# Performance work log

Hardware: AMD Instinct MI355X
Metric: run time of the kernel (lower is better)

## Reference

```python
import jax, jax.numpy as jnp
import numpy as np

D = 1024          # d_model == d_memory
N_LAYERS = 4      # memory MLP depth
EPS = 1e-5        # LayerNorm epsilon (no scale/bias in original)


def _layernorm(x):
    mu = jnp.mean(x, axis=-1, keepdims=True)
    var = jnp.var(x, axis=-1, keepdims=True)
    return (x - mu) * jax.lax.rsqrt(var + EPS)


def setup_inputs() -> dict:
    key = jax.random.key(0)
    ks = jax.random.split(key, 8)
    x = jax.random.normal(ks[0], (4, 4096, D), dtype=jnp.float32)
    # projection params (normal std 0.02, zero bias, matching flax init)
    wq = jax.random.normal(ks[1], (D, D), dtype=jnp.float32) * 0.02
    bq = jnp.zeros((D,), dtype=jnp.float32)
    w_out = jax.random.normal(ks[2], (D, D), dtype=jnp.float32) * 0.02
    b_out = jnp.zeros((D,), dtype=jnp.float32)
    # memory MLP: 4 layers, all D x D (d_in = d_hidden = d_out = D), stacked
    mlp_w = jax.random.normal(ks[3], (N_LAYERS, D, D), dtype=jnp.float32) * 0.02
    mlp_b = jnp.zeros((N_LAYERS, D), dtype=jnp.float32)
    return {"x": x, "wq": wq, "bq": bq, "mlp_w": mlp_w, "mlp_b": mlp_b,
            "w_out": w_out, "b_out": b_out}


def reference(x, wq, bq, mlp_w, mlp_b, w_out, b_out):
    # retrieve(): y = W_out( M*(LN(W_Q(x))) + straight-through(q_norm) )
    q = jnp.einsum("bsd,de->bse", x, wq) + bq
    q_norm = _layernorm(q)
    # memory MLP weights get stop_gradient in the original
    mw = jax.lax.stop_gradient(mlp_w)
    mb = jax.lax.stop_gradient(mlp_b)
    h = q_norm
    for i in range(N_LAYERS):
        h = jnp.einsum("bsd,de->bse", h, mw[i]) + mb[i]
        if i < N_LAYERS - 1:
            h = jax.nn.silu(h)
    # straight-through trick: zero in the forward, passes grad to q_norm
    out = h + (q_norm - jax.lax.stop_gradient(q_norm))
    return jnp.einsum("bsd,de->bse", out, w_out) + b_out
```

## Files before the change

### kernel.cpp

```cpp
#include <hip/hip_runtime.h>
#include <hip/hip_bf16.h>
#include <math.h>

#define D_MODEL 1024
#define DD (1024 * 1024)

typedef unsigned short ushort_t;
using short8 = __attribute__((ext_vector_type(8))) short;
using f32x4  = __attribute__((ext_vector_type(4))) float;

#define ACT_NONE 0
#define ACT_SILU 1

__device__ __forceinline__ float bf2f(ushort_t u) {
    return __uint_as_float(((unsigned int)u) << 16);
}
__device__ __forceinline__ ushort_t f2bf(float f) {
    unsigned int x = __float_as_uint(f);
    x += 0x7fffu + ((x >> 16) & 1u);
    return (ushort_t)(x >> 16);
}

#define GL2LDS(gp, lp)                                                         \
    __builtin_amdgcn_global_load_lds(                                          \
        (const __attribute__((address_space(1))) void*)(gp),                   \
        (__attribute__((address_space(3))) void*)(lp), 16, 0, 0)

template <int ACT, int OUTF32, int BIASF>
__global__ __launch_bounds__(256) void gemm_bf16(
    const ushort_t* __restrict__ A,
    const ushort_t* __restrict__ Bt,
    const float* __restrict__ bias,
    void* __restrict__ Cv, int M)
{
    constexpr int K = 1024, N = 1024;
    __shared__ ushort_t As[128 * 32];
    __shared__ ushort_t Bs[128 * 32];

    const int tid  = threadIdx.x;
    const int lane = tid & 63;
    const int wave = tid >> 6;
    const int quad = lane >> 4;
    const int lr   = lane & 15;
    const int bm   = blockIdx.x;
    const int bn   = blockIdx.y;
    const int wm   = (wave >> 1) * 64;
    const int wn   = (wave & 1) * 64;

    f32x4 acc[4][4];
#pragma unroll
    for (int i = 0; i < 4; i++)
#pragma unroll
        for (int j = 0; j < 4; j++) acc[i][j] = (f32x4){0.f, 0.f, 0.f, 0.f};

    int ci0 = tid, ci1 = tid + 256;
    int am0 = ci0 >> 2, akc0 = (ci0 & 3) ^ ((am0 >> 1) & 3);
    int am1 = ci1 >> 2, akc1 = (ci1 & 3) ^ ((am1 >> 1) & 3);
    const ushort_t* Ab = A + (size_t)(bm * 128) * K;
    const ushort_t* Bb = Bt + (size_t)(bn * 128) * K;

    for (int k0 = 0; k0 < K; k0 += 32) {
        GL2LDS(Ab + (size_t)am0 * K + k0 + akc0 * 8, As + ci0 * 8);
        GL2LDS(Ab + (size_t)am1 * K + k0 + akc1 * 8, As + ci1 * 8);
        GL2LDS(Bb + (size_t)am0 * K + k0 + akc0 * 8, Bs + ci0 * 8);
        GL2LDS(Bb + (size_t)am1 * K + k0 + akc1 * 8, Bs + ci1 * 8);
        __syncthreads();

        short8 af[4], bfr[4];
#pragma unroll
        for (int t = 0; t < 4; t++) {
            int m = wm + t * 16 + lr;
            af[t] = *(const short8*)(As + m * 32 + ((quad ^ ((m >> 1) & 3)) * 8));
            int n = wn + t * 16 + lr;
            bfr[t] = *(const short8*)(Bs + n * 32 + ((quad ^ ((n >> 1) & 3)) * 8));
        }
#pragma unroll
        for (int mt = 0; mt < 4; mt++)
#pragma unroll
            for (int nt = 0; nt < 4; nt++)
                acc[mt][nt] = __builtin_amdgcn_mfma_f32_16x16x32_bf16(
                    af[mt], bfr[nt], acc[mt][nt], 0, 0, 0);
        __syncthreads();
    }

    float bv[4];
#pragma unroll
    for (int nt = 0; nt < 4; nt++)
        bv[nt] = BIASF ? bias[bn * 128 + wn + nt * 16 + lr] : 0.f;

#pragma unroll
    for (int mt = 0; mt < 4; mt++) {
#pragma unroll
        for (int nt = 0; nt < 4; nt++) {
            const int col = bn * 128 + wn + nt * 16 + lr;
#pragma unroll
            for (int r = 0; r < 4; r++) {
                const int row = bm * 128 + wm + mt * 16 + quad * 4 + r;
                float v = acc[mt][nt][r] + bv[nt];
                if (ACT == ACT_SILU) v = v / (1.f + __expf(-v));
                if (OUTF32)
                    ((float*)Cv)[(size_t)row * N + col] = v;
                else
                    ((ushort_t*)Cv)[(size_t)row * N + col] = f2bf(v);
            }
        }
    }
}

__global__ __launch_bounds__(256) void layernorm_bf16(ushort_t* __restrict__ X)
{
    const int row = blockIdx.x;
    const int tid = threadIdx.x;
    ushort_t* x = X + (size_t)row * D_MODEL + tid * 4;

    uint2 u = *(uint2*)x;
    float a = bf2f(u.x & 0xffff), b = bf2f(u.x >> 16);
    float c = bf2f(u.y & 0xffff), d = bf2f(u.y >> 16);
    float s = a + b + c + d;
    float ss = a * a + b * b + c * c + d * d;

#pragma unroll
    for (int off = 32; off > 0; off >>= 1) {
        s += __shfl_down(s, off);
        ss += __shfl_down(ss, off);
    }
    __shared__ float sbuf[4], ssbuf[4];
    const int wave = tid >> 6;
    if ((tid & 63) == 0) { sbuf[wave] = s; ssbuf[wave] = ss; }
    __syncthreads();
    const float S = sbuf[0] + sbuf[1] + sbuf[2] + sbuf[3];
    const float SS = ssbuf[0] + ssbuf[1] + ssbuf[2] + ssbuf[3];
    const float mu = S * (1.f / D_MODEL);
    const float var = SS * (1.f / D_MODEL) - mu * mu;
    const float r = rsqrtf(var + 1e-5f);

    a = (a - mu) * r; b = (b - mu) * r; c = (c - mu) * r; d = (d - mu) * r;
    u.x = (unsigned)f2bf(a) | ((unsigned)f2bf(b) << 16);
    u.y = (unsigned)f2bf(c) | ((unsigned)f2bf(d) << 16);
    *(uint2*)x = u;
}

__global__ __launch_bounds__(256) void prep_all(
    const float* __restrict__ wq, const float* __restrict__ mlp_w,
    const float* __restrict__ w_out, const float* __restrict__ x,
    const float* __restrict__ b3, const float* __restrict__ bout,
    ushort_t* __restrict__ wt, ushort_t* __restrict__ Q,
    float* __restrict__ bf, int nxblk)
{
    const int blk = blockIdx.x;
    const int tid = threadIdx.x;

    if (blk < 6144) {
        const int z = blk >> 10;
        const int t = blk & 1023;
        const int k0 = (t >> 5) * 32;
        const int n0 = (t & 31) * 32;
        const int r = tid >> 5;
        const int c = tid & 31;

        if (z == 5) {
            const float* src = mlp_w + (size_t)3 * DD;
            ushort_t* dst = wt + (size_t)5 * DD;
#pragma unroll
            for (int i = 0; i < 4; i++) {
                size_t idx = (size_t)(k0 + r + 8 * i) * D_MODEL + n0 + c;
                dst[idx] = f2bf(src[idx]);
            }
            return;
        }
        const float* src = (z == 0) ? wq : (z < 4) ? (mlp_w + (size_t)(z - 1) * DD) : w_out;
        ushort_t* dst = wt + (size_t)z * DD;
        __shared__ float tile[32][33];
#pragma unroll
        for (int i = 0; i < 4; i++)
            tile[r + 8 * i][c] = src[(size_t)(k0 + r + 8 * i) * D_MODEL + n0 + c];
        __syncthreads();
#pragma unroll
        for (int i = 0; i < 4; i++)
            dst[(size_t)(n0 + r + 8 * i) * D_MODEL + k0 + c] = f2bf(tile[c][r + 8 * i]);
        return;
    }
    if (blk < 6144 + nxblk) {
        int i = (blk - 6144) * 256 + tid;
        const float4* p = (const float4*)(x + (size_t)i * 8);
        float4 v0 = p[0], v1 = p[1];
        union { ushort_t u[8]; uint4 v; } pk;
        pk.u[0] = f2bf(v0.x); pk.u[1] = f2bf(v0.y);
        pk.u[2] = f2bf(v0.z); pk.u[3] = f2bf(v0.w);
        pk.u[4] = f2bf(v1.x); pk.u[5] = f2bf(v1.y);
        pk.u[6] = f2bf(v1.z); pk.u[7] = f2bf(v1.w);
        *(uint4*)(Q + (size_t)i * 8) = pk.v;
        return;
    }
    {
        const int b = blk - 6144 - nxblk;
        const int n = b * 32 + (tid & 31);
        const int kg = tid >> 5;
        float s = 0.f;
        for (int k = kg * 128; k < (kg + 1) * 128; k++)
            s = fmaf(b3[k], w_out[(size_t)k * D_MODEL + n], s);
        __shared__ float red[8][32];
        red[kg][tid & 31] = s;
        __syncthreads();
        if (kg == 0) {
            float t = 0.f;
#pragma unroll
            for (int j = 0; j < 8; j++) t += red[j][tid & 31];
            bf[n] = t + bout[n];
        }
    }
}

extern "C" void kernel_launch(void* const* d_in, const int* in_sizes, int n_in,
                              void* d_out, int out_size, void* d_ws, size_t ws_size,
                              hipStream_t stream)
{
    const float* x     = (const float*)d_in[0];
    const float* wq    = (const float*)d_in[1];
    const float* bq    = (const float*)d_in[2];
    const float* mlp_w = (const float*)d_in[3];
    const float* mlp_b = (const float*)d_in[4];
    const float* w_out = (const float*)d_in[5];
    const float* b_out = (const float*)d_in[6];

    const int D = D_MODEL;
    const int M = in_sizes[0] / D;

    ushort_t* wt  = (ushort_t*)d_ws;
    ushort_t* w3b = wt + (size_t)5 * DD;
    ushort_t* wtF = wt + (size_t)6 * DD;
    ushort_t* Q   = wt + (size_t)7 * DD;
    float*    bf  = (float*)(Q + (size_t)M * D);
    ushort_t* P   = (ushort_t*)d_out;

    const int nxblk = M * D / 2048;
    prep_all<<<6144 + nxblk + 32, 256, 0, stream>>>(
        wq, mlp_w, w_out, x, mlp_b + 3 * D, b_out, wt, Q, bf, nxblk);
    gemm_bf16<ACT_NONE, 0, 0><<<dim3(8, 8), 256, 0, stream>>>(
        wt + (size_t)4 * DD, w3b, nullptr, wtF, 1024);

    dim3 grid(M / 128, D / 128);
    gemm_bf16<ACT_NONE, 0, 1><<<grid, 256, 0, stream>>>(Q, wt + (size_t)0 * DD, bq, P, M);
    layernorm_bf16<<<M, 256, 0, stream>>>(P);
    gemm_bf16<ACT_SILU, 0, 1><<<grid, 256, 0, stream>>>(P, wt + (size_t)1 * DD, mlp_b + 0 * D, Q, M);
    gemm_bf16<ACT_SILU, 0, 1><<<grid, 256, 0, stream>>>(Q, wt + (size_t)2 * DD, mlp_b + 1 * D, P, M);
    gemm_bf16<ACT_SILU, 0, 1><<<grid, 256, 0, stream>>>(P, wt + (size_t)3 * DD, mlp_b + 2 * D, Q, M);
    gemm_bf16<ACT_NONE, 1, 1><<<grid, 256, 0, stream>>>(Q, wtF, bf, d_out, M);
}
```

Baseline: 423.7 us.

## Add 256x256-tile 512-thread GEMM with 4-stage LDS pipeline for main chain

Adds a new GEMM kernel that computes 256x256 output tiles with 8 waves. It uses a 4-deep ring of LDS stages filled by direct global-to-LDS loads, interleaves MFMA phases with barriers and setprio, and swizzles the LDS layout. The goal is more data reuse per loaded byte and better overlap of loads with matrix math than the 128x128 kernel gives. The 5 large GEMMs use it when M is a multiple of 256. The cost is fewer blocks (M/256 x 4, which is 256 here for M=16384, roughly one per CU), a large accumulator register footprint, and more LDS, all of which risk lower occupancy.

```diff
diff --git a/kernel.cpp b/kernel.cpp
--- a/kernel.cpp
+++ b/kernel.cpp
@@ -25,6 +25,172 @@
     __builtin_amdgcn_global_load_lds(                                          \
         (const __attribute__((address_space(1))) void*)(gp),                   \
         (__attribute__((address_space(3))) void*)(lp), 16, 0, 0)
+
+template <int ACT, int OUTF32, int BIASF>
+__global__ __launch_bounds__(512, 2) void gemm256(
+    const ushort_t* __restrict__ A,
+    const ushort_t* __restrict__ Bt,
+    const float* __restrict__ bias,
+    void* __restrict__ Cv, int M)
+{
+    constexpr int K = 1024, N = 1024;
+    constexpr int NU = K / 32;
+    __shared__ ushort_t lds[4 * 16384];
+
+    const int tid  = threadIdx.x;
+    const int lane = tid & 63;
+    const int wave = tid >> 6;
+    const int quad = lane >> 4;
+    const int lr   = lane & 15;
+    const int wm   = wave >> 2;
+    const int wn   = wave & 3;
+    const int bm   = blockIdx.x;
+    const int bn   = blockIdx.y;
+
+    const ushort_t* Ab = A  + (size_t)bm * 256 * K;
+    const ushort_t* Bb = Bt + (size_t)bn * 256 * K;
+
+    const int sg    = (tid & 3) ^ ((tid >> 3) & 3);
+    const size_t s0 = (size_t)(tid >> 2) * K + (size_t)sg * 8;
+    const size_t s1 = s0 + (size_t)128 * K;
+    const int d0 = tid * 8;
+    const int d1 = tid * 8 + 4096;
+
+    const int chk  = quad ^ ((lr >> 1) & 3);
+    const int aoff = (wm * 128 + lr) * 32 + chk * 8;
+    const int boff = (wn * 64  + lr) * 32 + chk * 8;
+
+    f32x4 acc[8][4];
+#pragma unroll
+    for (int i = 0; i < 8; i++)
+#pragma unroll
+        for (int j = 0; j < 4; j++) acc[i][j] = (f32x4){0.f, 0.f, 0.f, 0.f};
+
+#define SA256(su) do { const int b_ = ((su) & 3) * 16384;                      \
+        GL2LDS(Ab + s0 + (su) * 32, lds + b_ + d0);                            \
+        GL2LDS(Ab + s1 + (su) * 32, lds + b_ + d1); } while (0)
+#define SB256(su) do { const int b_ = ((su) & 3) * 16384 + 8192;               \
+        GL2LDS(Bb + s0 + (su) * 32, lds + b_ + d0);                           \
+        GL2LDS(Bb + s1 + (su) * 32, lds + b_ + d1); } while (0)
+
+    SA256(0); SB256(0);
+    SA256(1); SB256(1);
+    SA256(2); SB256(2);
+    asm volatile("s_waitcnt vmcnt(4)" ::: "memory");
+    __builtin_amdgcn_s_barrier();
+
+    short8 afr[4], bfr[4];
+#pragma unroll
+    for (int u = 0; u < NU; u += 2) {
+        {
+            const ushort_t* Ax = lds + (u & 3) * 16384;
+            const ushort_t* Bx = Ax + 8192;
+#pragma unroll
+            for (int t = 0; t < 4; t++)
+                bfr[t] = *(const short8*)(Bx + boff + t * 512);
+#pragma unroll
+            for (int t = 0; t < 4; t++)
+                afr[t] = *(const short8*)(Ax + aoff + t * 512);
+            if (u + 3 < NU) SA256(u + 3);
+            __builtin_amdgcn_s_barrier();
+            asm volatile("s_waitcnt lgkmcnt(0)" ::: "memory");
+            __builtin_amdgcn_sched_barrier(0);
+            __builtin_amdgcn_s_setprio(1);
+#pragma unroll
+            for (int mt = 0; mt < 4; mt++)
+#pragma unroll
+                for (int nt = 0; nt < 4; nt++)
+                    acc[mt][nt] = __builtin_amdgcn_mfma_f32_16x16x32_bf16(
+                        afr[mt], bfr[nt], acc[mt][nt], 0, 0, 0);
+            __builtin_amdgcn_s_setprio(0);
+            __builtin_amdgcn_s_barrier();
+#pragma unroll
+            for (int t = 0; t < 4; t++)
+                afr[t] = *(const short8*)(Ax + aoff + (4 + t) * 512);
+            if (u + 3 < NU) SB256(u + 3);
+            __builtin_amdgcn_s_barrier();
+            asm volatile("s_waitcnt lgkmcnt(0)" ::: "memory");
+            __builtin_amdgcn_sched_barrier(0);
+            __builtin_amdgcn_s_setprio(1);
+#pragma unroll
+            for (int mt = 0; mt < 4; mt++)
+#pragma unroll
+                for (int nt = 0; nt < 4; nt++)
+                    acc[mt + 4][nt] = __builtin_amdgcn_mfma_f32_16x16x32_bf16(
+                        afr[mt], bfr[nt], acc[mt + 4][nt], 0, 0, 0);
+            __builtin_amdgcn_s_setprio(0);
+            __builtin_amdgcn_s_barrier();
+        }
+        {
+            const ushort_t* Ax = lds + ((u + 1) & 3) * 16384;
+            const ushort_t* Bx = Ax + 8192;
+#pragma unroll
+            for (int t = 0; t < 4; t++)
+                bfr[t] = *(const short8*)(Bx + boff + t * 512);
+#pragma unroll
+            for (int t = 0; t < 4; t++)
+                afr[t] = *(const short8*)(Ax + aoff + t * 512);
+            if (u + 4 < NU) SA256(u + 4);
+            __builtin_amdgcn_s_barrier();
+            asm volatile("s_waitcnt lgkmcnt(0)" ::: "memory");
+            __builtin_amdgcn_sched_barrier(0);
+            __builtin_amdgcn_s_setprio(1);
+#pragma unroll
+            for (int mt = 0; mt < 4; mt++)
+#pragma unroll
+                for (int nt = 0; nt < 4; nt++)
+                    acc[mt][nt] = __builtin_amdgcn_mfma_f32_16x16x32_bf16(
+                        afr[mt], bfr[nt], acc[mt][nt], 0, 0, 0);
+            __builtin_amdgcn_s_setprio(0);
+            __builtin_amdgcn_s_barrier();
+#pragma unroll
+            for (int t = 0; t < 4; t++)
+                afr[t] = *(const short8*)(Ax + aoff + (4 + t) * 512);
+            if (u + 4 < NU) SB256(u + 4);
+            __builtin_amdgcn_s_barrier();
+            asm volatile("s_waitcnt lgkmcnt(0)" ::: "memory");
+            __builtin_amdgcn_sched_barrier(0);
+            __builtin_amdgcn_s_setprio(1);
+#pragma unroll
+            for (int mt = 0; mt < 4; mt++)
+#pragma unroll
+                for (int nt = 0; nt < 4; nt++)
+                    acc[mt + 4][nt] = __builtin_amdgcn_mfma_f32_16x16x32_bf16(
+                        afr[mt], bfr[nt], acc[mt + 4][nt], 0, 0, 0);
+            __builtin_amdgcn_s_setprio(0);
+            if (u + 4 >= NU)
+                asm volatile("s_waitcnt vmcnt(0)" ::: "memory");
+            else
+                asm volatile("s_waitcnt vmcnt(4)" ::: "memory");
+            __builtin_amdgcn_s_barrier();
+        }
+    }
+#undef SA256
+#undef SB256
+
+    float bv[4];
+#pragma unroll
+    for (int nt = 0; nt < 4; nt++)
+        bv[nt] = BIASF ? bias[bn * 256 + wn * 64 + nt * 16 + lr] : 0.f;
+
+#pragma unroll
+    for (int mt = 0; mt < 8; mt++) {
+#pragma unroll
+        for (int nt = 0; nt < 4; nt++) {
+            const int col = bn * 256 + wn * 64 + nt * 16 + lr;
+#pragma unroll
+            for (int r = 0; r < 4; r++) {
+                const int row = bm * 256 + wm * 128 + mt * 16 + quad * 4 + r;
+                float v = acc[mt][nt][r] + bv[nt];
+                if (ACT == ACT_SILU) v = v / (1.f + __expf(-v));
+                if (OUTF32)
+                    ((float*)Cv)[(size_t)row * N + col] = v;
+                else
+                    ((ushort_t*)Cv)[(size_t)row * N + col] = f2bf(v);
+            }
+        }
+    }
+}
 
 template <int ACT, int OUTF32, int BIASF>
 __global__ __launch_bounds__(256) void gemm_bf16(
@@ -239,11 +405,21 @@
     gemm_bf16<ACT_NONE, 0, 0><<<dim3(8, 8), 256, 0, stream>>>(
         wt + (size_t)4 * DD, w3b, nullptr, wtF, 1024);
 
-    dim3 grid(M / 128, D / 128);
-    gemm_bf16<ACT_NONE, 0, 1><<<grid, 256, 0, stream>>>(Q, wt + (size_t)0 * DD, bq, P, M);
-    layernorm_bf16<<<M, 256, 0, stream>>>(P);
-    gemm_bf16<ACT_SILU, 0, 1><<<grid, 256, 0, stream>>>(P, wt + (size_t)1 * DD, mlp_b + 0 * D, Q, M);
-    gemm_bf16<ACT_SILU, 0, 1><<<grid, 256, 0, stream>>>(Q, wt + (size_t)2 * DD, mlp_b + 1 * D, P, M);
-    gemm_bf16<ACT_SILU, 0, 1><<<grid, 256, 0, stream>>>(P, wt + (size_t)3 * DD, mlp_b + 2 * D, Q, M);
-    gemm_bf16<ACT_NONE, 1, 1><<<grid, 256, 0, stream>>>(Q, wtF, bf, d_out, M);
-}
+    if ((M & 255) == 0) {
+        dim3 grid(M / 256, D / 256);
+        gemm256<ACT_NONE, 0, 1><<<grid, 512, 0, stream>>>(Q, wt + (size_t)0 * DD, bq, P, M);
+        layernorm_bf16<<<M, 256, 0, stream>>>(P);
+        gemm256<ACT_SILU, 0, 1><<<grid, 512, 0, stream>>>(P, wt + (size_t)1 * DD, mlp_b + 0 * D, Q, M);
+        gemm256<ACT_SILU, 0, 1><<<grid, 512, 0, stream>>>(Q, wt + (size_t)2 * DD, mlp_b + 1 * D, P, M);
+        gemm256<ACT_SILU, 0, 1><<<grid, 512, 0, stream>>>(P, wt + (size_t)3 * DD, mlp_b + 2 * D, Q, M);
+        gemm256<ACT_NONE, 1, 1><<<grid, 512, 0, stream>>>(Q, wtF, bf, d_out, M);
+    } else {
+        dim3 grid(M / 128, D / 128);
+        gemm_bf16<ACT_NONE, 0, 1><<<grid, 256, 0, stream>>>(Q, wt + (size_t)0 * DD, bq, P, M);
+        layernorm_bf16<<<M, 256, 0, stream>>>(P);
+        gemm_bf16<ACT_SILU, 0, 1><<<grid, 256, 0, stream>>>(P, wt + (size_t)1 * DD, mlp_b + 0 * D, Q, M);
+        gemm_bf16<ACT_SILU, 0, 1><<<grid, 256, 0, stream>>>(Q, wt + (size_t)2 * DD, mlp_b + 1 * D, P, M);
+        gemm_bf16<ACT_SILU, 0, 1><<<grid, 256, 0, stream>>>(P, wt + (size_t)3 * DD, mlp_b + 2 * D, Q, M);
+        gemm_bf16<ACT_NONE, 1, 1><<<grid, 256, 0, stream>>>(Q, wtF, bf, d_out, M);
+    }
+}
```

Result: faster. 356.0 us (-16.0%).

## Add 256x256-tile multistage MFMA GEMM for the main activation GEMMs

Applied to the files above, without the earlier changes.

Adds a new GEMM kernel that computes 256x256 output tiles with 512 threads, using 32x32x16 bf16 MFMAs. Operands stream through a 4-stage LDS ring via direct global-to-LDS loads with swizzled addressing. Fragment reads are double-buffered and interleaved with MFMA issue under explicit waitcnt, sched_barrier and setprio control. The aim is more data reuse per tile and better overlap of memory with compute than the 128x128 kernel. In exchange it uses 128KB of LDS and many registers, leaving about one block per CU. With 256 blocks that gives a single wave of work with no latency hiding from other blocks. The old kernel stays as a fallback when M is not a multiple of 256.

```diff
diff --git a/kernel.cpp b/kernel.cpp
--- a/kernel.cpp
+++ b/kernel.cpp
@@ -8,6 +8,7 @@
 typedef unsigned short ushort_t;
 using short8 = __attribute__((ext_vector_type(8))) short;
 using f32x4  = __attribute__((ext_vector_type(4))) float;
+using f32x16 = __attribute__((ext_vector_type(16))) float;
 
 #define ACT_NONE 0
 #define ACT_SILU 1
@@ -25,6 +26,160 @@
     __builtin_amdgcn_global_load_lds(                                          \
         (const __attribute__((address_space(1))) void*)(gp),                   \
         (__attribute__((address_space(3))) void*)(lp), 16, 0, 0)
+
+template <int ACT, int OUTF32, int BIASF>
+__global__ __launch_bounds__(512, 2) void gemm256(
+    const ushort_t* __restrict__ A,
+    const ushort_t* __restrict__ Bt,
+    const float* __restrict__ bias,
+    void* __restrict__ Cv, int M)
+{
+    constexpr int K = 1024, N = 1024;
+    constexpr int NU = K / 32;
+    __shared__ ushort_t lds[4 * 16384];
+
+    const int tid  = threadIdx.x;
+    const int lane = tid & 63;
+    const int wave = tid >> 6;
+    const int l31  = lane & 31;
+    const int hi   = lane >> 5;
+    const int wm   = wave >> 2;
+    const int wn   = wave & 3;
+    const int bm   = blockIdx.x;
+    const int bn   = blockIdx.y;
+
+    const ushort_t* Ab = A  + (size_t)bm * 256 * K;
+    const ushort_t* Bb = Bt + (size_t)bn * 256 * K;
+
+    const int sg    = (tid & 3) ^ ((tid >> 3) & 3);
+    const size_t s0 = (size_t)(tid >> 2) * K + (size_t)sg * 8;
+    const size_t s1 = s0 + (size_t)128 * K;
+    const int d0 = tid * 8;
+    const int d1 = tid * 8 + 4096;
+
+    const int x0    = (l31 >> 1) & 3;
+    const int c0    = hi ^ x0;
+    const int arow  = wm * 128 + l31;
+    const int brow  = wn * 64 + l31;
+    const int aoff0 = arow * 32 + c0 * 8;
+    const int aoff1 = arow * 32 + (c0 ^ 2) * 8;
+    const int boff0 = brow * 32 + c0 * 8;
+    const int boff1 = brow * 32 + (c0 ^ 2) * 8;
+
+    short8 afrX[8], afrY[8], bfr[4];
+    f32x16 acc[4][2];
+#pragma unroll
+    for (int i = 0; i < 4; i++)
+#pragma unroll
+        for (int j = 0; j < 2; j++)
+#pragma unroll
+            for (int r = 0; r < 16; r++) acc[i][j][r] = 0.f;
+
+#define SA(v) do { const int b_ = ((v) & 3) * 16384;                           \
+        GL2LDS(Ab + s0 + (v) * 32, lds + b_ + d0);                             \
+        GL2LDS(Ab + s1 + (v) * 32, lds + b_ + d1); } while (0)
+#define SB(v) do { const int b_ = ((v) & 3) * 16384 + 8192;                    \
+        GL2LDS(Bb + s0 + (v) * 32, lds + b_ + d0);                             \
+        GL2LDS(Bb + s1 + (v) * 32, lds + b_ + d1); } while (0)
+#define RA_(dst, v) do { const ushort_t* p_ = lds + ((v) & 3) * 16384;         \
+        dst[0] = *(const short8*)(p_ + aoff0);                                 \
+        dst[1] = *(const short8*)(p_ + aoff0 + 1024);                          \
+        dst[2] = *(const short8*)(p_ + aoff0 + 2048);                          \
+        dst[3] = *(const short8*)(p_ + aoff0 + 3072);                          \
+        dst[4] = *(const short8*)(p_ + aoff1);                                 \
+        dst[5] = *(const short8*)(p_ + aoff1 + 1024);                          \
+        dst[6] = *(const short8*)(p_ + aoff1 + 2048);                          \
+        dst[7] = *(const short8*)(p_ + aoff1 + 3072); } while (0)
+#define RB_(v) do { const ushort_t* p_ = lds + ((v) & 3) * 16384 + 8192;       \
+        bfr[0] = *(const short8*)(p_ + boff0);                                 \
+        bfr[1] = *(const short8*)(p_ + boff0 + 1024);                          \
+        bfr[2] = *(const short8*)(p_ + boff1);                                 \
+        bfr[3] = *(const short8*)(p_ + boff1 + 1024); } while (0)
+
+#define MFMA8_KS0(CUR) do {                                                    \
+        _Pragma("unroll")                                                      \
+        for (int mt = 0; mt < 4; mt++) {                                       \
+            acc[mt][0] = __builtin_amdgcn_mfma_f32_32x32x16_bf16(              \
+                CUR[mt], bfr[0], acc[mt][0], 0, 0, 0);                         \
+            acc[mt][1] = __builtin_amdgcn_mfma_f32_32x32x16_bf16(              \
+                CUR[mt], bfr[1], acc[mt][1], 0, 0, 0);                         \
+        } } while (0)
+#define MFMA8_KS1(CUR) do {                                                    \
+        _Pragma("unroll")                                                      \
+        for (int mt = 0; mt < 4; mt++) {                                       \
+            acc[mt][0] = __builtin_amdgcn_mfma_f32_32x32x16_bf16(              \
+                CUR[4 + mt], bfr[2], acc[mt][0], 0, 0, 0);                     \
+            acc[mt][1] = __builtin_amdgcn_mfma_f32_32x32x16_bf16(              \
+                CUR[4 + mt], bfr[3], acc[mt][1], 0, 0, 0);                     \
+        } } while (0)
+
+#define UNIT(u, CUR, NXT) do {                                                 \
+        if ((u) == NU - 2) asm volatile("s_waitcnt vmcnt(0)" ::: "memory");    \
+        else               asm volatile("s_waitcnt vmcnt(4)" ::: "memory");    \
+        __builtin_amdgcn_s_barrier();                                          \
+        if ((u) + 3 < NU) { SA((u) + 3); SB((u) + 3); }                        \
+        asm volatile("s_waitcnt lgkmcnt(2)" ::: "memory");                     \
+        __builtin_amdgcn_sched_barrier(0);                                     \
+        __builtin_amdgcn_s_setprio(1);                                         \
+        MFMA8_KS0(CUR);                                                        \
+        __builtin_amdgcn_s_setprio(0);                                         \
+        if ((u) + 1 < NU) RA_(NXT, (u) + 1);                                   \
+        if ((u) + 1 < NU)                                                      \
+            asm volatile("s_waitcnt lgkmcnt(8)" ::: "memory");                 \
+        else                                                                   \
+            asm volatile("s_waitcnt lgkmcnt(0)" ::: "memory");                 \
+        __builtin_amdgcn_sched_barrier(0);                                     \
+        __builtin_amdgcn_s_setprio(1);                                         \
+        MFMA8_KS1(CUR);                                                        \
+        __builtin_amdgcn_s_setprio(0);                                         \
+        if ((u) + 1 < NU) RB_((u) + 1);                                        \
+    } while (0)
+
+    SA(0); SB(0);
+    SA(1); SB(1);
+    SA(2); SB(2);
+    asm volatile("s_waitcnt vmcnt(8)" ::: "memory");
+    __builtin_amdgcn_s_barrier();
+    RA_(afrX, 0);
+    RB_(0);
+
+#pragma unroll
+    for (int uu = 0; uu < NU; uu += 2) {
+        UNIT(uu,     afrX, afrY);
+        UNIT(uu + 1, afrY, afrX);
+    }
+#undef SA
+#undef SB
+#undef RA_
+#undef RB_
+#undef MFMA8_KS0
+#undef MFMA8_KS1
+#undef UNIT
+
+    float bv[2];
+#pragma unroll
+    for (int nt = 0; nt < 2; nt++)
+        bv[nt] = BIASF ? bias[bn * 256 + wn * 64 + nt * 32 + l31] : 0.f;
+
+#pragma unroll
+    for (int mt = 0; mt < 4; mt++) {
+#pragma unroll
+        for (int nt = 0; nt < 2; nt++) {
+            const int col = bn * 256 + wn * 64 + nt * 32 + l31;
+#pragma unroll
+            for (int r = 0; r < 16; r++) {
+                const int row = bm * 256 + wm * 128 + mt * 32 +
+                                (r & 3) + 8 * (r >> 2) + 4 * hi;
+                float v = acc[mt][nt][r] + bv[nt];
+                if (ACT == ACT_SILU) v = v / (1.f + __expf(-v));
+                if (OUTF32)
+                    ((float*)Cv)[(size_t)row * N + col] = v;
+                else
+                    ((ushort_t*)Cv)[(size_t)row * N + col] = f2bf(v);
+            }
+        }
+    }
+}
 
 template <int ACT, int OUTF32, int BIASF>
 __global__ __launch_bounds__(256) void gemm_bf16(
@@ -239,11 +394,21 @@
     gemm_bf16<ACT_NONE, 0, 0><<<dim3(8, 8), 256, 0, stream>>>(
         wt + (size_t)4 * DD, w3b, nullptr, wtF, 1024);
 
-    dim3 grid(M / 128, D / 128);
-    gemm_bf16<ACT_NONE, 0, 1><<<grid, 256, 0, stream>>>(Q, wt + (size_t)0 * DD, bq, P, M);
-    layernorm_bf16<<<M, 256, 0, stream>>>(P);
-    gemm_bf16<ACT_SILU, 0, 1><<<grid, 256, 0, stream>>>(P, wt + (size_t)1 * DD, mlp_b + 0 * D, Q, M);
-    gemm_bf16<ACT_SILU, 0, 1><<<grid, 256, 0, stream>>>(Q, wt + (size_t)2 * DD, mlp_b + 1 * D, P, M);
-    gemm_bf16<ACT_SILU, 0, 1><<<grid, 256, 0, stream>>>(P, wt + (size_t)3 * DD, mlp_b + 2 * D, Q, M);
-    gemm_bf16<ACT_NONE, 1, 1><<<grid, 256, 0, stream>>>(Q, wtF, bf, d_out, M);
-}
+    if ((M & 255) == 0) {
+        dim3 grid(M / 256, D / 256);
+        gemm256<ACT_NONE, 0, 1><<<grid, 512, 0, stream>>>(Q, wt + (size_t)0 * DD, bq, P, M);
+        layernorm_bf16<<<M, 256, 0, stream>>>(P);
+        gemm256<ACT_SILU, 0, 1><<<grid, 512, 0, stream>>>(P, wt + (size_t)1 * DD, mlp_b + 0 * D, Q, M);
+        gemm256<ACT_SILU, 0, 1><<<grid, 512, 0, stream>>>(Q, wt + (size_t)2 * DD, mlp_b + 1 * D, P, M);
+        gemm256<ACT_SILU, 0, 1><<<grid, 512, 0, stream>>>(P, wt + (size_t)3 * DD, mlp_b + 2 * D, Q, M);
+        gemm256<ACT_NONE, 1, 1><<<grid, 512, 0, stream>>>(Q, wtF, bf, d_out, M);
+    } else {
+        dim3 grid(M / 128, D / 128);
+        gemm_bf16<ACT_NONE, 0, 1><<<grid, 256, 0, stream>>>(Q, wt + (size_t)0 * DD, bq, P, M);
+        layernorm_bf16<<<M, 256, 0, stream>>>(P);
+        gemm_bf16<ACT_SILU, 0, 1><<<grid, 256, 0, stream>>>(P, wt + (size_t)1 * DD, mlp_b + 0 * D, Q, M);
+        gemm_bf16<ACT_SILU, 0, 1><<<grid, 256, 0, stream>>>(Q, wt + (size_t)2 * DD, mlp_b + 1 * D, P, M);
+        gemm_bf16<ACT_SILU, 0, 1><<<grid, 256, 0, stream>>>(P, wt + (size_t)3 * DD, mlp_b + 2 * D, Q, M);
+        gemm_bf16<ACT_NONE, 1, 1><<<grid, 256, 0, stream>>>(Q, wtF, bf, d_out, M);
+    }
+}
```

Result: faster. 375.1 us (-11.5%).

## Add 256x256-tile, 512-thread GEMM with double-buffered LDS and phased MFMA schedule

Applied to the files above, without the earlier changes.

Adds a new GEMM kernel that uses 256x256 output tiles with 8 waves per block (each wave computing 128x64). It double-buffers 64-wide K slices in LDS via direct global-to-LDS loads with XOR swizzling, and interleaves LDS reads, prefetch and MFMA in four barrier-separated phases with raised wave priority. The goal is more operand reuse per byte loaded and overlap of global loads with compute across the five 4096x4-row GEMMs. In exchange it holds a large register accumulator set and 128 KB of LDS per block, so occupancy is lower and the grid is smaller, which may underfill the CUs.

```diff
diff --git a/kernel.cpp b/kernel.cpp
--- a/kernel.cpp
+++ b/kernel.cpp
@@ -25,6 +25,135 @@
     __builtin_amdgcn_global_load_lds(                                          \
         (const __attribute__((address_space(1))) void*)(gp),                   \
         (__attribute__((address_space(3))) void*)(lp), 16, 0, 0)
+
+template <int ACT, int OUTF32, int BIASF>
+__global__ __launch_bounds__(512, 2) void gemm256(
+    const ushort_t* __restrict__ A,
+    const ushort_t* __restrict__ Bt,
+    const float* __restrict__ bias,
+    void* __restrict__ Cv, int M)
+{
+    constexpr int K = 1024, N = 1024;
+    constexpr int NT = K / 64;
+    __shared__ ushort_t lds[2 * 32768];
+
+    const int tid  = threadIdx.x;
+    const int lane = tid & 63;
+    const int wave = tid >> 6;
+    const int quad = lane >> 4;
+    const int lr   = lane & 15;
+    const int wm   = wave >> 2;
+    const int wn   = wave & 3;
+    const int bm   = blockIdx.x;
+    const int bn   = blockIdx.y;
+
+    const int sg    = (tid & 3) ^ ((tid >> 3) & 3);
+    const size_t sA = (size_t)(bm * 256 + (tid >> 2)) * K + (size_t)sg * 8;
+    const size_t sB = (size_t)(bn * 256 + (tid >> 2)) * K + (size_t)sg * 8;
+    const int dd    = tid * 8;
+
+    const int chk  = quad ^ ((lr >> 1) & 3);
+    const int aoff = (wm * 128 + lr) * 32 + chk * 8;
+    const int boff = 16384 + (wn * 64 + lr) * 32 + chk * 8;
+
+    short8 av[2][2], bv8[4][2];
+    f32x4 acc[8][4];
+#pragma unroll
+    for (int i = 0; i < 8; i++)
+#pragma unroll
+        for (int j = 0; j < 4; j++) acc[i][j] = (f32x4){0.f, 0.f, 0.f, 0.f};
+
+#define STAGE8(kt, bufs) do { const int b_ = (bufs) * 32768;                   \
+        const size_t ko_ = (size_t)(kt) * 64;                                  \
+        GL2LDS(A  + sA + ko_,               lds + b_ + dd);                    \
+        GL2LDS(A  + sA + ko_ + 131072,      lds + b_ + 4096  + dd);            \
+        GL2LDS(A  + sA + ko_ + 32,          lds + b_ + 8192  + dd);            \
+        GL2LDS(A  + sA + ko_ + 131072 + 32, lds + b_ + 12288 + dd);            \
+        GL2LDS(Bt + sB + ko_,               lds + b_ + 16384 + dd);            \
+        GL2LDS(Bt + sB + ko_ + 131072,      lds + b_ + 20480 + dd);            \
+        GL2LDS(Bt + sB + ko_ + 32,          lds + b_ + 24576 + dd);            \
+        GL2LDS(Bt + sB + ko_ + 131072 + 32, lds + b_ + 28672 + dd);            \
+    } while (0)
+
+#define RDA(p, cb) do {                                                        \
+        av[0][0] = *(const short8*)(lds + (cb) + aoff + (2*(p)) * 512);        \
+        av[0][1] = *(const short8*)(lds + (cb) + 8192 + aoff + (2*(p)) * 512); \
+        av[1][0] = *(const short8*)(lds + (cb) + aoff + (2*(p)+1) * 512);      \
+        av[1][1] = *(const short8*)(lds + (cb) + 8192 + aoff + (2*(p)+1)*512); \
+    } while (0)
+
+#define RDB(cb) do {                                                           \
+        _Pragma("unroll")                                                      \
+        for (int nt_ = 0; nt_ < 4; nt_++) {                                    \
+            bv8[nt_][0] = *(const short8*)(lds + (cb) + boff + nt_ * 512);     \
+            bv8[nt_][1] = *(const short8*)(lds + (cb) + 8192 + boff + nt_*512);\
+        } } while (0)
+
+#define PHASE(t, p) do {                                                       \
+        const int cb_ = ((t) & 1) * 32768;                                     \
+        RDA(p, cb_);                                                           \
+        if ((p) == 0) {                                                        \
+            RDB(cb_);                                                          \
+            if ((t) + 1 < NT) STAGE8((t) + 1, ((t) + 1) & 1);                  \
+        }                                                                      \
+        if ((p) == 3 && (t) + 1 < NT)                                          \
+            asm volatile("s_waitcnt vmcnt(0)" ::: "memory");                   \
+        __builtin_amdgcn_s_barrier();                                          \
+        asm volatile("s_waitcnt lgkmcnt(0)" ::: "memory");                     \
+        __builtin_amdgcn_sched_barrier(0);                                     \
+        __builtin_amdgcn_s_setprio(1);                                         \
+        _Pragma("unroll")                                                      \
+        for (int m2 = 0; m2 < 2; m2++)                                         \
+            _Pragma("unroll")                                                  \
+            for (int nt_ = 0; nt_ < 4; nt_++) {                                \
+                acc[2*(p)+m2][nt_] = __builtin_amdgcn_mfma_f32_16x16x32_bf16(  \
+                    av[m2][0], bv8[nt_][0], acc[2*(p)+m2][nt_], 0, 0, 0);      \
+                acc[2*(p)+m2][nt_] = __builtin_amdgcn_mfma_f32_16x16x32_bf16(  \
+                    av[m2][1], bv8[nt_][1], acc[2*(p)+m2][nt_], 0, 0, 0);      \
+            }                                                                  \
+        __builtin_amdgcn_s_setprio(0);                                         \
+        __builtin_amdgcn_s_barrier();                                          \
+    } while (0)
+
+    STAGE8(0, 0);
+    asm volatile("s_waitcnt vmcnt(0)" ::: "memory");
+    __builtin_amdgcn_s_barrier();
+
+#pragma unroll
+    for (int t = 0; t < NT; ++t) {
+        PHASE(t, 0);
+        PHASE(t, 1);
+        PHASE(t, 2);
+        PHASE(t, 3);
+    }
+#undef STAGE8
+#undef RDA
+#undef RDB
+#undef PHASE
+
+    float bv[4];
+#pragma unroll
+    for (int nt = 0; nt < 4; nt++)
+        bv[nt] = BIASF ? bias[bn * 256 + wn * 64 + nt * 16 + lr] : 0.f;
+
+#pragma unroll
+    for (int mt = 0; mt < 8; mt++) {
+#pragma unroll
+        for (int nt = 0; nt < 4; nt++) {
+            const int col = bn * 256 + wn * 64 + nt * 16 + lr;
+#pragma unroll
+            for (int r = 0; r < 4; r++) {
+                const int row = bm * 256 + wm * 128 + mt * 16 + quad * 4 + r;
+                float v = acc[mt][nt][r] + bv[nt];
+                if (ACT == ACT_SILU) v = v / (1.f + __expf(-v));
+                if (OUTF32)
+                    ((float*)Cv)[(size_t)row * N + col] = v;
+                else
+                    ((ushort_t*)Cv)[(size_t)row * N + col] = f2bf(v);
+            }
+        }
+    }
+}
 
 template <int ACT, int OUTF32, int BIASF>
 __global__ __launch_bounds__(256) void gemm_bf16(
@@ -239,11 +368,21 @@
     gemm_bf16<ACT_NONE, 0, 0><<<dim3(8, 8), 256, 0, stream>>>(
         wt + (size_t)4 * DD, w3b, nullptr, wtF, 1024);
 
-    dim3 grid(M / 128, D / 128);
-    gemm_bf16<ACT_NONE, 0, 1><<<grid, 256, 0, stream>>>(Q, wt + (size_t)0 * DD, bq, P, M);
-    layernorm_bf16<<<M, 256, 0, stream>>>(P);
-    gemm_bf16<ACT_SILU, 0, 1><<<grid, 256, 0, stream>>>(P, wt + (size_t)1 * DD, mlp_b + 0 * D, Q, M);
-    gemm_bf16<ACT_SILU, 0, 1><<<grid, 256, 0, stream>>>(Q, wt + (size_t)2 * DD, mlp_b + 1 * D, P, M);
-    gemm_bf16<ACT_SILU, 0, 1><<<grid, 256, 0, stream>>>(P, wt + (size_t)3 * DD, mlp_b + 2 * D, Q, M);
-    gemm_bf16<ACT_NONE, 1, 1><<<grid, 256, 0, stream>>>(Q, wtF, bf, d_out, M);
-}
+    if ((M & 255) == 0) {
+        dim3 grid(M / 256, D / 256);
+        gemm256<ACT_NONE, 0, 1><<<grid, 512, 0, stream>>>(Q, wt + (size_t)0 * DD, bq, P, M);
+        layernorm_bf16<<<M, 256, 0, stream>>>(P);
+        gemm256<ACT_SILU, 0, 1><<<grid, 512, 0, stream>>>(P, wt + (size_t)1 * DD, mlp_b + 0 * D, Q, M);
+        gemm256<ACT_SILU, 0, 1><<<grid, 512, 0, stream>>>(Q, wt + (size_t)2 * DD, mlp_b + 1 * D, P, M);
+        gemm256<ACT_SILU, 0, 1><<<grid, 512, 0, stream>>>(P, wt + (size_t)3 * DD, mlp_b + 2 * D, Q, M);
+        gemm256<ACT_NONE, 1, 1><<<grid, 512, 0, stream>>>(Q, wtF, bf, d_out, M);
+    } else {
+        dim3 grid(M / 128, D / 128);
+        gemm_bf16<ACT_NONE, 0, 1><<<grid, 256, 0, stream>>>(Q, wt + (size_t)0 * DD, bq, P, M);
+        layernorm_bf16<<<M, 256, 0, stream>>>(P);
+        gemm_bf16<ACT_SILU, 0, 1><<<grid, 256, 0, stream>>>(P, wt + (size_t)1 * DD, mlp_b + 0 * D, Q, M);
+        gemm_bf16<ACT_SILU, 0, 1><<<grid, 256, 0, stream>>>(Q, wt + (size_t)2 * DD, mlp_b + 1 * D, P, M);
+        gemm_bf16<ACT_SILU, 0, 1><<<grid, 256, 0, stream>>>(P, wt + (size_t)3 * DD, mlp_b + 2 * D, Q, M);
+        gemm_bf16<ACT_NONE, 1, 1><<<grid, 256, 0, stream>>>(Q, wtF, bf, d_out, M);
+    }
+}
```

Result: faster. 385.2 us (-9.1%).
